# Optimization experiments

Hardware: AMD Instinct MI355X
Metric: run time of the kernel (lower is better)

## Reference

```python
import jax, jax.numpy as jnp
import numpy as np

N = 8192
IN_F = 256
OUT_F = 128
E = 262144
NEG = -9e15


def setup_inputs() -> dict:
    key = jax.random.key(0)
    ks = jax.random.split(key, 12)
    glorot = lambda k, shp: jax.random.uniform(k, shp, jnp.float32,
                                               -jnp.sqrt(6.0 / (shp[0] + shp[1])),
                                               jnp.sqrt(6.0 / (shp[0] + shp[1])))
    return {
        "h_context": jax.random.normal(ks[0], (N, IN_F), jnp.float32),
        "h_structure": jax.random.normal(ks[1], (N, IN_F), jnp.float32),
        "edge_index": jax.random.randint(ks[2], (2, E), 0, N, jnp.int64),
        "Wc_w": glorot(ks[3], (OUT_F, IN_F)),
        "Wc_b": jnp.zeros((OUT_F,), jnp.float32),
        "Ws_w": glorot(ks[4], (OUT_F, IN_F)),
        "Ws_b": jnp.zeros((OUT_F,), jnp.float32),
        "ac_w": glorot(ks[5], (1, 2 * OUT_F)),
        "as_w": glorot(ks[6], (1, 2 * OUT_F)),
        "Ws_coff": jax.random.normal(ks[7], (1, 1), jnp.float32) * 1.414,
        "Wc_coff": jax.random.normal(ks[8], (1, 1), jnp.float32) * 1.414,
    }


def _pair_scores(h, a_w):
    # GAT trick: score[i,j] = leaky_relu(a1 . h[i] + a2 . h[j])
    F_out = h.shape[1]
    s_src = h @ a_w[0, :F_out]   # [N]
    s_dst = h @ a_w[0, F_out:]   # [N]
    return jax.nn.leaky_relu(s_src[:, None] + s_dst[None, :], 0.01)  # [N, N]


def reference(h_context, h_structure, edge_index, Wc_w, Wc_b, Ws_w, Ws_b,
              ac_w, as_w, Ws_coff, Wc_coff):
    hc = h_context @ Wc_w.T + Wc_b                      # [N, F]
    alpha_c = _pair_scores(hc, ac_w)                    # [N, N]
    hs = jax.nn.softmax(h_structure, axis=1) @ Ws_w.T + Ws_b
    alpha_s = _pair_scores(hs, as_w)                    # [N, N]
    alpha = jnp.abs(Ws_coff[0, 0]) * alpha_c + jnp.abs(Wc_coff[0, 0]) * alpha_s
    n = h_structure.shape[0]
    adj = jnp.zeros((n, n), bool).at[edge_index[0], edge_index[1]].set(True)
    attention = jnp.where(adj, alpha, NEG)
    attention = jax.nn.softmax(attention, axis=1)
    # dropout omitted (eval mode / deterministic reference)
    return attention @ hc
```

## Files before the change

### kernel.cpp

```cpp
#include <hip/hip_runtime.h>
#include <hip/hip_bf16.h>
#include <math.h>

#define N_NODES 8192
#define IN_FEAT 256
#define OUT_FEAT 128
#define WORDS_PER_ROW (N_NODES / 64)
#define CAP 512
#define M_TILE 16

typedef unsigned long long u64;
typedef float v4f __attribute__((ext_vector_type(4)));
typedef short s8v __attribute__((ext_vector_type(8)));
typedef short s4v __attribute__((ext_vector_type(4)));

__device__ __forceinline__ float wred_sum_b(float v) {
    #pragma unroll
    for (int o = 32; o > 0; o >>= 1) v += __shfl_xor(v, o, 64);
    return v;
}
__device__ __forceinline__ float wred_max_b(float v) {
    #pragma unroll
    for (int o = 32; o > 0; o >>= 1) v = fmaxf(v, __shfl_xor(v, o, 64));
    return v;
}

__device__ __forceinline__ void bsplit(float x, unsigned short& hi, unsigned short& lo) {
    unsigned int xb = __float_as_uint(x);
    hi = (unsigned short)(xb >> 16);
    float lof = x - __uint_as_float(xb & 0xFFFF0000u);
    lo = (unsigned short)(__float_as_uint(lof) >> 16);
}

__global__ __launch_bounds__(256) void prep_w(
    const float* __restrict__ Wc, const float* __restrict__ Ws,
    unsigned short* __restrict__ wchi, unsigned short* __restrict__ wclo,
    unsigned short* __restrict__ wshi, unsigned short* __restrict__ wslo)
{
    int i = blockIdx.x * 256 + threadIdx.x;
    unsigned short h, l;
    bsplit(Wc[i], h, l); wchi[i] = h; wclo[i] = l;
    bsplit(Ws[i], h, l); wshi[i] = h; wslo[i] = l;
}

__global__ __launch_bounds__(256) void node_feats(
    const float* __restrict__ hctx, const float* __restrict__ hstr,
    const unsigned short* __restrict__ wchi, const unsigned short* __restrict__ wclo,
    const unsigned short* __restrict__ wshi, const unsigned short* __restrict__ wslo,
    const float* __restrict__ Wcb, const float* __restrict__ Wsb,
    const float* __restrict__ acw, const float* __restrict__ asw,
    float* __restrict__ hc,
    float* __restrict__ csrc, float* __restrict__ cdst,
    float* __restrict__ ssrc, float* __restrict__ sdst)
{
    __shared__ unsigned short aCh[M_TILE][264], aCl[M_TILE][264];
    __shared__ unsigned short aSh[M_TILE][264], aSl[M_TILE][264];
    __shared__ float invsh[M_TILE];
    __shared__ float hcT[M_TILE][132];
    __shared__ float hsT[M_TILE][132];

    const int t = threadIdx.x;
    const int w = t >> 6, ln = t & 63;
    const int r0 = blockIdx.x * M_TILE;

    #pragma unroll
    for (int j = 0; j < 4; j++) {
        int c = t + 256 * j;
        int r = c >> 6;
        int k = (c & 63) * 4;
        const float4 x = *(const float4*)(hctx + (size_t)(r0 + r) * IN_FEAT + k);
        unsigned short h0, h1, h2, h3, l0, l1, l2, l3;
        bsplit(x.x, h0, l0); bsplit(x.y, h1, l1);
        bsplit(x.z, h2, l2); bsplit(x.w, h3, l3);
        s4v hv = { (short)h0, (short)h1, (short)h2, (short)h3 };
        s4v lv = { (short)l0, (short)l1, (short)l2, (short)l3 };
        *(s4v*)&aCh[r][k] = hv;
        *(s4v*)&aCl[r][k] = lv;
    }

    #pragma unroll
    for (int rr = 0; rr < 4; rr++) {
        int r = w * 4 + rr;
        const float* srow = hstr + (size_t)(r0 + r) * IN_FEAT;
        float x0 = srow[ln], x1 = srow[ln + 64], x2 = srow[ln + 128], x3 = srow[ln + 192];
        float mx = wred_max_b(fmaxf(fmaxf(x0, x1), fmaxf(x2, x3)));
        float e0 = __expf(x0 - mx), e1 = __expf(x1 - mx);
        float e2 = __expf(x2 - mx), e3 = __expf(x3 - mx);
        float s = wred_sum_b(e0 + e1 + e2 + e3);
        if (ln == 0) invsh[r] = 1.0f / s;
        unsigned short h, l;
        bsplit(e0, h, l); aSh[r][ln]       = h; aSl[r][ln]       = l;
        bsplit(e1, h, l); aSh[r][ln + 64]  = h; aSl[r][ln + 64]  = l;
        bsplit(e2, h, l); aSh[r][ln + 128] = h; aSl[r][ln + 128] = l;
        bsplit(e3, h, l); aSh[r][ln + 192] = h; aSl[r][ln + 192] = l;
    }
    __syncthreads();

    const int m = ln & 15, q = ln >> 4;
    const int nA = (w << 5) + m, nB = nA + 16;
    const unsigned short* bchA = wchi + nA * IN_FEAT;
    const unsigned short* bchB = wchi + nB * IN_FEAT;
    const unsigned short* bclA = wclo + nA * IN_FEAT;
    const unsigned short* bclB = wclo + nB * IN_FEAT;
    const unsigned short* bshA = wshi + nA * IN_FEAT;
    const unsigned short* bshB = wshi + nB * IN_FEAT;
    const unsigned short* bslA = wslo + nA * IN_FEAT;
    const unsigned short* bslB = wslo + nB * IN_FEAT;

    v4f aC0 = {0.f,0.f,0.f,0.f}, aC1 = {0.f,0.f,0.f,0.f};
    v4f aS0 = {0.f,0.f,0.f,0.f}, aS1 = {0.f,0.f,0.f,0.f};

    #pragma unroll
    for (int ks = 0; ks < 8; ks++) {
        int ko = ks * 32 + q * 8;
        s8v ach = *(const s8v*)&aCh[m][ko];
        s8v acl = *(const s8v*)&aCl[m][ko];
        s8v ash = *(const s8v*)&aSh[m][ko];
        s8v asl = *(const s8v*)&aSl[m][ko];
        s8v bch0 = *(const s8v*)(bchA + ko);
        s8v bch1 = *(const s8v*)(bchB + ko);
        s8v bcl0 = *(const s8v*)(bclA + ko);
        s8v bcl1 = *(const s8v*)(bclB + ko);
        s8v bsh0 = *(const s8v*)(bshA + ko);
        s8v bsh1 = *(const s8v*)(bshB + ko);
        s8v bsl0 = *(const s8v*)(bslA + ko);
        s8v bsl1 = *(const s8v*)(bslB + ko);

        aC0 = __builtin_amdgcn_mfma_f32_16x16x32_bf16(acl, bch0, aC0, 0, 0, 0);
        aC0 = __builtin_amdgcn_mfma_f32_16x16x32_bf16(ach, bcl0, aC0, 0, 0, 0);
        aC0 = __builtin_amdgcn_mfma_f32_16x16x32_bf16(ach, bch0, aC0, 0, 0, 0);
        aC1 = __builtin_amdgcn_mfma_f32_16x16x32_bf16(acl, bch1, aC1, 0, 0, 0);
        aC1 = __builtin_amdgcn_mfma_f32_16x16x32_bf16(ach, bcl1, aC1, 0, 0, 0);
        aC1 = __builtin_amdgcn_mfma_f32_16x16x32_bf16(ach, bch1, aC1, 0, 0, 0);
        aS0 = __builtin_amdgcn_mfma_f32_16x16x32_bf16(asl, bsh0, aS0, 0, 0, 0);
        aS0 = __builtin_amdgcn_mfma_f32_16x16x32_bf16(ash, bsl0, aS0, 0, 0, 0);
        aS0 = __builtin_amdgcn_mfma_f32_16x16x32_bf16(ash, bsh0, aS0, 0, 0, 0);
        aS1 = __builtin_amdgcn_mfma_f32_16x16x32_bf16(asl, bsh1, aS1, 0, 0, 0);
        aS1 = __builtin_amdgcn_mfma_f32_16x16x32_bf16(ash, bsl1, aS1, 0, 0, 0);
        aS1 = __builtin_amdgcn_mfma_f32_16x16x32_bf16(ash, bsh1, aS1, 0, 0, 0);
    }

    const float cbA = Wcb[nA], cbB = Wcb[nB];
    const float sbA = Wsb[nA], sbB = Wsb[nB];
    #pragma unroll
    for (int p = 0; p < 4; p++) {
        int row = q * 4 + p;
        float iv = invsh[row];
        hcT[row][nA] = aC0[p] + cbA;
        hcT[row][nB] = aC1[p] + cbB;
        hsT[row][nA] = aS0[p] * iv + sbA;
        hsT[row][nB] = aS1[p] * iv + sbB;
    }
    __syncthreads();

    #pragma unroll
    for (int j = 0; j < 8; j++) {
        int f = t + 256 * j;
        int r = f >> 7, c = f & 127;
        hc[(size_t)(r0 + r) * OUT_FEAT + c] = hcT[r][c];
    }

    float a0 = acw[ln], a0b = acw[ln + 64], a1 = acw[128 + ln], a1b = acw[192 + ln];
    float b0 = asw[ln], b0b = asw[ln + 64], b1 = asw[128 + ln], b1b = asw[192 + ln];
    #pragma unroll
    for (int rr = 0; rr < 4; rr++) {
        int r = w + rr * 4;
        float c0 = hcT[r][ln], c1 = hcT[r][ln + 64];
        float s0 = hsT[r][ln], s1 = hsT[r][ln + 64];
        float v0 = wred_sum_b(c0 * a0 + c1 * a0b);
        float v1 = wred_sum_b(c0 * a1 + c1 * a1b);
        float v2 = wred_sum_b(s0 * b0 + s1 * b0b);
        float v3 = wred_sum_b(s0 * b1 + s1 * b1b);
        if (ln == 0) {
            csrc[r0 + r] = v0; cdst[r0 + r] = v1;
            ssrc[r0 + r] = v2; sdst[r0 + r] = v3;
        }
    }
}

__global__ __launch_bounds__(256) void scatter_edges(
    const int* __restrict__ ei, int E, u64* __restrict__ bmp)
{
    __shared__ int is64sh;
    int pv = 0;
    if (threadIdx.x < 32) pv = ei[2 * threadIdx.x + 1];
    u64 nz = __ballot(pv != 0);
    if (threadIdx.x == 0) is64sh = (nz == 0) ? 1 : 0;
    __syncthreads();
    const int is64 = is64sh;

    int e = blockIdx.x * 256 + threadIdx.x;
    if (e >= E) return;
    int s, d;
    if (is64) { s = ei[2 * e]; d = ei[2 * E + 2 * e]; }
    else      { s = ei[e];     d = ei[E + e]; }
    if ((unsigned)s < N_NODES && (unsigned)d < N_NODES)
        atomicOr(&bmp[(size_t)s * WORDS_PER_ROW + (d >> 6)], 1ull << (d & 63));
}

__global__ __launch_bounds__(128) void attn(
    const u64* __restrict__ bmp,
    const float* __restrict__ hc,
    const float* __restrict__ csrc, const float* __restrict__ cdst,
    const float* __restrict__ ssrc, const float* __restrict__ sdst,
    const float* __restrict__ wscoff, const float* __restrict__ wccoff,
    float* __restrict__ out)
{
    __shared__ int   jlist[CAP];
    __shared__ float plist[CAP];
    __shared__ float redM[2];
    __shared__ float redS[2];
    __shared__ int   cnt_sh;

    const int i = blockIdx.x;
    const int t = threadIdx.x;
    const int wv = t >> 6, ln = t & 63;
    if (t == 0) cnt_sh = 0;
    __syncthreads();

    const float wS = fabsf(wscoff[0]);
    const float wC = fabsf(wccoff[0]);
    const float cs = csrc[i];
    const float ss = ssrc[i];

    u64 w = bmp[(size_t)i * WORDS_PER_ROW + t];
    while (w) {
        int b = __ffsll(w) - 1;
        w &= (w - 1);
        int j = t * 64 + b;
        float ac  = cs + cdst[j];
        float as_ = ss + sdst[j];
        ac  = (ac  > 0.0f) ? ac  : 0.01f * ac;
        as_ = (as_ > 0.0f) ? as_ : 0.01f * as_;
        float a = wS * ac + wC * as_;
        int idx = atomicAdd(&cnt_sh, 1);
        if (idx < CAP) { jlist[idx] = j; plist[idx] = a; }
    }
    __syncthreads();
    int cnt = cnt_sh; if (cnt > CAP) cnt = CAP;

    if (cnt == 0) {
        float acc = 0.0f;
        for (int j = 0; j < N_NODES; j++) acc += hc[(size_t)j * OUT_FEAT + t];
        out[(size_t)i * OUT_FEAT + t] = acc / (float)N_NODES;
        return;
    }

    float lm = -1e30f;
    for (int k = t; k < cnt; k += 128) lm = fmaxf(lm, plist[k]);
    lm = wred_max_b(lm);
    if (ln == 0) redM[wv] = lm;
    __syncthreads();
    float m = fmaxf(redM[0], redM[1]);

    float ls = 0.0f;
    for (int k = t; k < cnt; k += 128) {
        float p = __expf(plist[k] - m);
        plist[k] = p;
        ls += p;
    }
    ls = wred_sum_b(ls);
    if (ln == 0) redS[wv] = ls;
    __syncthreads();
    float inv = 1.0f / (redS[0] + redS[1]);

    float acc = 0.0f;
    int k = 0;
    for (; k + 4 <= cnt; k += 4) {
        int   j0 = jlist[k],   j1 = jlist[k+1], j2 = jlist[k+2], j3 = jlist[k+3];
        float p0 = plist[k],   p1 = plist[k+1], p2 = plist[k+2], p3 = plist[k+3];
        acc += p0 * hc[(size_t)j0 * OUT_FEAT + t]
             + p1 * hc[(size_t)j1 * OUT_FEAT + t]
             + p2 * hc[(size_t)j2 * OUT_FEAT + t]
             + p3 * hc[(size_t)j3 * OUT_FEAT + t];
    }
    for (; k < cnt; k++) acc += plist[k] * hc[(size_t)jlist[k] * OUT_FEAT + t];

    out[(size_t)i * OUT_FEAT + t] = acc * inv;
}

extern "C" void kernel_launch(void* const* d_in, const int* in_sizes, int n_in,
                              void* d_out, int out_size, void* d_ws, size_t ws_size,
                              hipStream_t stream)
{
    const float* hctx = (const float*)d_in[0];
    const float* hstr = (const float*)d_in[1];
    const int*   ei   = (const int*)d_in[2];
    const float* Wc   = (const float*)d_in[3];
    const float* Wcb  = (const float*)d_in[4];
    const float* Ws   = (const float*)d_in[5];
    const float* Wsb  = (const float*)d_in[6];
    const float* acw  = (const float*)d_in[7];
    const float* asw  = (const float*)d_in[8];
    const float* wsco = (const float*)d_in[9];
    const float* wcco = (const float*)d_in[10];
    float* out = (float*)d_out;

    const int n2 = in_sizes[2];
    const int E  = (n2 == 4 * 262144) ? 262144 : n2 / 2;

    char* ws = (char*)d_ws;
    size_t off = 0;
    float* hc   = (float*)(ws + off); off += (size_t)N_NODES * OUT_FEAT * sizeof(float);
    float* csrc = (float*)(ws + off); off += (size_t)N_NODES * sizeof(float);
    float* cdst = (float*)(ws + off); off += (size_t)N_NODES * sizeof(float);
    float* ssrc = (float*)(ws + off); off += (size_t)N_NODES * sizeof(float);
    float* sdst = (float*)(ws + off); off += (size_t)N_NODES * sizeof(float);
    off = (off + 255) & ~(size_t)255;
    u64* bmp    = (u64*)(ws + off);   off += (size_t)N_NODES * WORDS_PER_ROW * sizeof(u64);
    unsigned short* wchi = (unsigned short*)(ws + off); off += OUT_FEAT * IN_FEAT * sizeof(unsigned short);
    unsigned short* wclo = (unsigned short*)(ws + off); off += OUT_FEAT * IN_FEAT * sizeof(unsigned short);
    unsigned short* wshi = (unsigned short*)(ws + off); off += OUT_FEAT * IN_FEAT * sizeof(unsigned short);
    unsigned short* wslo = (unsigned short*)(ws + off); off += OUT_FEAT * IN_FEAT * sizeof(unsigned short);

    hipMemsetAsync(bmp, 0, (size_t)N_NODES * WORDS_PER_ROW * sizeof(u64), stream);

    prep_w<<<128, 256, 0, stream>>>(Wc, Ws, wchi, wclo, wshi, wslo);
    node_feats<<<N_NODES / M_TILE, 256, 0, stream>>>(hctx, hstr, wchi, wclo, wshi, wslo,
                                                     Wcb, Wsb, acw, asw,
                                                     hc, csrc, cdst, ssrc, sdst);
    scatter_edges<<<(E + 255) / 256, 256, 0, stream>>>(ei, E, bmp);
    attn<<<N_NODES, 128, 0, stream>>>(bmp, hc, csrc, cdst, ssrc, sdst, wsco, wcco, out);
}
```

Measured before the change: 136.0 us.

## Fuse edge scatter into node_feats and process one attention row per wavefront

```diff
diff --git a/kernel.cpp b/kernel.cpp
--- a/kernel.cpp
+++ b/kernel.cpp
@@ -6,7 +6,7 @@
 #define IN_FEAT 256
 #define OUT_FEAT 128
 #define WORDS_PER_ROW (N_NODES / 64)
-#define CAP 512
+#define CAPW 256
 #define M_TILE 16
 
 typedef unsigned long long u64;
@@ -49,6 +49,7 @@
     const unsigned short* __restrict__ wshi, const unsigned short* __restrict__ wslo,
     const float* __restrict__ Wcb, const float* __restrict__ Wsb,
     const float* __restrict__ acw, const float* __restrict__ asw,
+    const int* __restrict__ ei, int E, u64* __restrict__ bmp,
     float* __restrict__ hc,
     float* __restrict__ csrc, float* __restrict__ cdst,
     float* __restrict__ ssrc, float* __restrict__ sdst)
@@ -62,6 +63,19 @@
     const int t = threadIdx.x;
     const int w = t >> 6, ln = t & 63;
     const int r0 = blockIdx.x * M_TILE;
+
+    {
+        int pv = ei[2 * (ln & 31) + 1];
+        u64 nz = __ballot(pv != 0);
+        const int is64 = (nz == 0);
+        for (int e = blockIdx.x * 256 + t; e < E; e += 512 * 256) {
+            int s, d;
+            if (is64) { s = ei[2 * e]; d = ei[2 * E + 2 * e]; }
+            else      { s = ei[e];     d = ei[E + e]; }
+            if ((unsigned)s < N_NODES && (unsigned)d < N_NODES)
+                atomicOr(&bmp[(size_t)s * WORDS_PER_ROW + (d >> 6)], 1ull << (d & 63));
+        }
+    }
 
     #pragma unroll
     for (int j = 0; j < 4; j++) {
@@ -178,27 +192,7 @@
     }
 }
 
-__global__ __launch_bounds__(256) void scatter_edges(
-    const int* __restrict__ ei, int E, u64* __restrict__ bmp)
-{
-    __shared__ int is64sh;
-    int pv = 0;
-    if (threadIdx.x < 32) pv = ei[2 * threadIdx.x + 1];
-    u64 nz = __ballot(pv != 0);
-    if (threadIdx.x == 0) is64sh = (nz == 0) ? 1 : 0;
-    __syncthreads();
-    const int is64 = is64sh;
-
-    int e = blockIdx.x * 256 + threadIdx.x;
-    if (e >= E) return;
-    int s, d;
-    if (is64) { s = ei[2 * e]; d = ei[2 * E + 2 * e]; }
-    else      { s = ei[e];     d = ei[E + e]; }
-    if ((unsigned)s < N_NODES && (unsigned)d < N_NODES)
-        atomicOr(&bmp[(size_t)s * WORDS_PER_ROW + (d >> 6)], 1ull << (d & 63));
-}
-
-__global__ __launch_bounds__(128) void attn(
+__global__ __launch_bounds__(256) void attn(
     const u64* __restrict__ bmp,
     const float* __restrict__ hc,
     const float* __restrict__ csrc, const float* __restrict__ cdst,
@@ -206,77 +200,93 @@
     const float* __restrict__ wscoff, const float* __restrict__ wccoff,
     float* __restrict__ out)
 {
-    __shared__ int   jlist[CAP];
-    __shared__ float plist[CAP];
-    __shared__ float redM[2];
-    __shared__ float redS[2];
-    __shared__ int   cnt_sh;
-
-    const int i = blockIdx.x;
-    const int t = threadIdx.x;
-    const int wv = t >> 6, ln = t & 63;
-    if (t == 0) cnt_sh = 0;
-    __syncthreads();
+    __shared__ int   jl[4][CAPW];
+    __shared__ float pl[4][CAPW];
+
+    const int w  = threadIdx.x >> 6;
+    const int ln = threadIdx.x & 63;
+    const int i  = blockIdx.x * 4 + w;
 
     const float wS = fabsf(wscoff[0]);
     const float wC = fabsf(wccoff[0]);
-    const float cs = csrc[i];
-    const float ss = ssrc[i];
-
-    u64 w = bmp[(size_t)i * WORDS_PER_ROW + t];
-    while (w) {
-        int b = __ffsll(w) - 1;
-        w &= (w - 1);
-        int j = t * 64 + b;
-        float ac  = cs + cdst[j];
-        float as_ = ss + sdst[j];
-        ac  = (ac  > 0.0f) ? ac  : 0.01f * ac;
-        as_ = (as_ > 0.0f) ? as_ : 0.01f * as_;
-        float a = wS * ac + wC * as_;
-        int idx = atomicAdd(&cnt_sh, 1);
-        if (idx < CAP) { jlist[idx] = j; plist[idx] = a; }
-    }
-    __syncthreads();
-    int cnt = cnt_sh; if (cnt > CAP) cnt = CAP;
+    const float cs = csrc[i], ss = ssrc[i];
+
+    ulonglong2 wv = *(const ulonglong2*)(bmp + (size_t)i * WORDS_PER_ROW + 2 * ln);
+    int c = __popcll(wv.x) + __popcll(wv.y);
+
+    int inc = c;
+    #pragma unroll
+    for (int o = 1; o < 64; o <<= 1) {
+        int y = __shfl_up(inc, o, 64);
+        if (ln >= o) inc += y;
+    }
+    int pre = inc - c;
+    int cnt = __shfl(inc, 63, 64);
+
+    int idx = pre;
+    #pragma unroll
+    for (int h = 0; h < 2; h++) {
+        u64 ww = (h == 0) ? wv.x : wv.y;
+        int jb = ln * 128 + h * 64;
+        while (ww) {
+            int b = __ffsll(ww) - 1; ww &= ww - 1;
+            int j = jb + b;
+            float ac  = cs + cdst[j];
+            float as_ = ss + sdst[j];
+            ac  = (ac  > 0.0f) ? ac  : 0.01f * ac;
+            as_ = (as_ > 0.0f) ? as_ : 0.01f * as_;
+            if (idx < CAPW) { jl[w][idx] = j; pl[w][idx] = wS * ac + wC * as_; }
+            idx++;
+        }
+    }
+    if (cnt > CAPW) cnt = CAPW;
+    __threadfence_block();
 
     if (cnt == 0) {
-        float acc = 0.0f;
-        for (int j = 0; j < N_NODES; j++) acc += hc[(size_t)j * OUT_FEAT + t];
-        out[(size_t)i * OUT_FEAT + t] = acc / (float)N_NODES;
+        float2 acc = {0.f, 0.f};
+        const float2* hc2 = (const float2*)hc;
+        for (int j = 0; j < N_NODES; j++) {
+            float2 h2 = hc2[(size_t)j * 64 + ln];
+            acc.x += h2.x; acc.y += h2.y;
+        }
+        float2 o2 = { acc.x / (float)N_NODES, acc.y / (float)N_NODES };
+        *(float2*)(out + (size_t)i * OUT_FEAT + 2 * ln) = o2;
         return;
     }
 
-    float lm = -1e30f;
-    for (int k = t; k < cnt; k += 128) lm = fmaxf(lm, plist[k]);
-    lm = wred_max_b(lm);
-    if (ln == 0) redM[wv] = lm;
-    __syncthreads();
-    float m = fmaxf(redM[0], redM[1]);
-
-    float ls = 0.0f;
-    for (int k = t; k < cnt; k += 128) {
-        float p = __expf(plist[k] - m);
-        plist[k] = p;
-        ls += p;
-    }
-    ls = wred_sum_b(ls);
-    if (ln == 0) redS[wv] = ls;
-    __syncthreads();
-    float inv = 1.0f / (redS[0] + redS[1]);
-
-    float acc = 0.0f;
+    float m = -1e30f;
+    for (int k = ln; k < cnt; k += 64) m = fmaxf(m, pl[w][k]);
+    m = wred_max_b(m);
+    float s = 0.0f;
+    for (int k = ln; k < cnt; k += 64) {
+        float p = __expf(pl[w][k] - m);
+        pl[w][k] = p;
+        s += p;
+    }
+    s = wred_sum_b(s);
+    float inv = 1.0f / s;
+    __threadfence_block();
+
+    const float2* hc2 = (const float2*)hc;
+    float2 acc = {0.f, 0.f};
     int k = 0;
     for (; k + 4 <= cnt; k += 4) {
-        int   j0 = jlist[k],   j1 = jlist[k+1], j2 = jlist[k+2], j3 = jlist[k+3];
-        float p0 = plist[k],   p1 = plist[k+1], p2 = plist[k+2], p3 = plist[k+3];
-        acc += p0 * hc[(size_t)j0 * OUT_FEAT + t]
-             + p1 * hc[(size_t)j1 * OUT_FEAT + t]
-             + p2 * hc[(size_t)j2 * OUT_FEAT + t]
-             + p3 * hc[(size_t)j3 * OUT_FEAT + t];
-    }
-    for (; k < cnt; k++) acc += plist[k] * hc[(size_t)jlist[k] * OUT_FEAT + t];
-
-    out[(size_t)i * OUT_FEAT + t] = acc * inv;
+        int   j0 = jl[w][k],   j1 = jl[w][k+1], j2 = jl[w][k+2], j3 = jl[w][k+3];
+        float p0 = pl[w][k],   p1 = pl[w][k+1], p2 = pl[w][k+2], p3 = pl[w][k+3];
+        float2 h0 = hc2[(size_t)j0 * 64 + ln];
+        float2 h1 = hc2[(size_t)j1 * 64 + ln];
+        float2 h2 = hc2[(size_t)j2 * 64 + ln];
+        float2 h3 = hc2[(size_t)j3 * 64 + ln];
+        acc.x += p0 * h0.x + p1 * h1.x + p2 * h2.x + p3 * h3.x;
+        acc.y += p0 * h0.y + p1 * h1.y + p2 * h2.y + p3 * h3.y;
+    }
+    for (; k < cnt; k++) {
+        float2 h0 = hc2[(size_t)jl[w][k] * 64 + ln];
+        float p0 = pl[w][k];
+        acc.x += p0 * h0.x; acc.y += p0 * h0.y;
+    }
+    float2 o2 = { acc.x * inv, acc.y * inv };
+    *(float2*)(out + (size_t)i * OUT_FEAT + 2 * ln) = o2;
 }
 
 extern "C" void kernel_launch(void* const* d_in, const int* in_sizes, int n_in,
@@ -317,8 +327,7 @@
 
     prep_w<<<128, 256, 0, stream>>>(Wc, Ws, wchi, wclo, wshi, wslo);
     node_feats<<<N_NODES / M_TILE, 256, 0, stream>>>(hctx, hstr, wchi, wclo, wshi, wslo,
-                                                     Wcb, Wsb, acw, asw,
+                                                     Wcb, Wsb, acw, asw, ei, E, bmp,
                                                      hc, csrc, cdst, ssrc, sdst);
-    scatter_edges<<<(E + 255) / 256, 256, 0, stream>>>(ei, E, bmp);
-    attn<<<N_NODES, 128, 0, stream>>>(bmp, hc, csrc, cdst, ssrc, sdst, wsco, wcco, out);
-}
+    attn<<<N_NODES / 4, 256, 0, stream>>>(bmp, hc, csrc, cdst, ssrc, sdst, wsco, wcco, out);
+}
```

Measured after the change: 130.3 us. -4.2%, faster.
